# Kernel tuning notes

Hardware: AMD Instinct MI355X
Metric: run time of the kernel (lower is better)

## Reference

```python
import jax, jax.numpy as jnp
import numpy as np

DIM = 768
HEADS = 12
HEAD_DIM = DIM // HEADS
SCALE = HEAD_DIM ** -0.5


def setup_inputs() -> dict:
    key = jax.random.key(0)
    k1, k2, k3, k4, k5 = jax.random.split(key, 5)
    B, N = 4, 2048
    x = jax.random.normal(k1, (B, N, DIM), dtype=jnp.float32)
    # qkv Linear: weight [3*dim, dim], bias [3*dim]
    w_qkv = jax.random.normal(k2, (3 * DIM, DIM), dtype=jnp.float32) * (DIM ** -0.5)
    b_qkv = jax.random.normal(k3, (3 * DIM,), dtype=jnp.float32) * 0.01
    # proj Linear: weight [dim, dim], bias [dim]
    w_proj = jax.random.normal(k4, (DIM, DIM), dtype=jnp.float32) * (DIM ** -0.5)
    b_proj = jax.random.normal(k5, (DIM,), dtype=jnp.float32) * 0.01
    return {"x": x, "w_qkv": w_qkv, "b_qkv": b_qkv, "w_proj": w_proj, "b_proj": b_proj}


def reference(x, w_qkv, b_qkv, w_proj, b_proj):
    B, N, C = x.shape
    qkv = (jnp.einsum('bnc,oc->bno', x, w_qkv) + b_qkv)
    qkv = qkv.reshape(B, N, 3, HEADS, HEAD_DIM).transpose(2, 0, 3, 1, 4)
    q, k, v = qkv[0], qkv[1], qkv[2]
    attn = jnp.einsum('bhqd,bhkd->bhqk', q, k) * SCALE
    attn = jax.nn.softmax(attn, axis=-1)
    out = jnp.einsum('bhqk,bhkd->bhqd', attn, v)  # [B, H, N, Dh]
    out = out.transpose(0, 2, 1, 3).reshape(B, N, C)
    # dropout is identity in eval mode
    return jnp.einsum('bnc,oc->bno', out, w_proj) + b_proj
```

## Files before the change

kernel.cpp:

```cpp
#include <hip/hip_runtime.h>
#include <hip/hip_bf16.h>

using bf16 = __hip_bfloat16;
typedef __bf16 bf16x8 __attribute__((ext_vector_type(8)));
typedef short short4v __attribute__((ext_vector_type(4)));
typedef short short8v __attribute__((ext_vector_type(8)));
typedef float float4v __attribute__((ext_vector_type(4)));

#define DIM   768
#define NH    12
#define HD    64
#define SEQ   2048
#define BATCH 4
#define TOK   (BATCH * SEQ)
#define SCALE_QL2E 0.18033688011112042f

#define NX  (TOK * DIM)
#define NWQ (3 * DIM * DIM)
#define NWP (DIM * DIM)

__device__ __forceinline__ short f2bf(float f) {
  union { bf16 h; short s; } u;
  u.h = __float2bfloat16(f);
  return u.s;
}

union frag8 { short4v h[2]; short8v s; bf16x8 b; unsigned u[4]; };

__device__ __forceinline__ void async_copy16(const bf16* g, short* l) {
  __builtin_amdgcn_global_load_lds(
      (const __attribute__((address_space(1))) unsigned int*)g,
      (__attribute__((address_space(3))) unsigned int*)l, 16, 0, 0);
}
__device__ __forceinline__ void async_copy4(const bf16* g, short* l) {
  __builtin_amdgcn_global_load_lds(
      (const __attribute__((address_space(1))) unsigned int*)g,
      (__attribute__((address_space(3))) unsigned int*)l, 4, 0, 0);
}

#define BARRIER __builtin_amdgcn_s_barrier()
#define LGKM0 asm volatile("s_waitcnt lgkmcnt(0)" ::: "memory")
#define VW0 asm volatile("s_waitcnt vmcnt(0)" ::: "memory")
#define NOSTG (void)0
#define NOVW  (void)0

__global__ void __launch_bounds__(256)
cvt3(const float* __restrict__ a, bf16* __restrict__ oa, long na,
     const float* __restrict__ b, bf16* __restrict__ ob, long nb,
     const float* __restrict__ c, bf16* __restrict__ oc, long nc) {
  const long i = ((long)blockIdx.x * 256 + threadIdx.x) * 8;
  const float* src; bf16* dst; long off;
  if (i < na)                { src = a; dst = oa; off = i; }
  else if (i < na + nb)      { src = b; dst = ob; off = i - na; }
  else if (i < na + nb + nc) { src = c; dst = oc; off = i - na - nb; }
  else return;
  const float4v x0 = *(const float4v*)(src + off);
  const float4v x1 = *(const float4v*)(src + off + 4);
  short8v r;
  r[0] = f2bf(x0[0]); r[1] = f2bf(x0[1]); r[2] = f2bf(x0[2]); r[3] = f2bf(x0[3]);
  r[4] = f2bf(x1[0]); r[5] = f2bf(x1[1]); r[6] = f2bf(x1[2]); r[7] = f2bf(x1[3]);
  *(short8v*)(dst + off) = r;
}

__device__ __forceinline__ void gemm_mainloop(const bf16* __restrict__ A,
                                              const bf16* __restrict__ B,
                                              short* As, short* Bs,
                                              float4v acc[4][4]) {
  const int t = threadIdx.x;
  const int w = t >> 6, l = t & 63, lr = l & 15, q = l >> 4;
  const int wr = ((w >> 1) << 6), wc = ((w & 1) << 6);

  const bf16* Ag = A + (t >> 2) * DIM + (t & 3) * 8;
  const bf16* Bg = B + (t >> 2) * DIM + (t & 3) * 8;

  for (int k0 = 0; k0 < DIM; k0 += 32) {
    __syncthreads();
    async_copy16(Ag,            &As[t * 8]);
    async_copy16(Ag + 64 * DIM, &As[2048 + t * 8]);
    async_copy16(Bg,            &Bs[t * 8]);
    async_copy16(Bg + 64 * DIM, &Bs[2048 + t * 8]);
    Ag += 32; Bg += 32;
    __syncthreads();

    bf16x8 af[4], bfv[4];
#pragma unroll
    for (int i = 0; i < 4; ++i)
      af[i] = *(const bf16x8*)&As[(wr + i * 16 + lr) * 32 + q * 8];
#pragma unroll
    for (int j = 0; j < 4; ++j)
      bfv[j] = *(const bf16x8*)&Bs[(wc + j * 16 + lr) * 32 + q * 8];
#pragma unroll
    for (int i = 0; i < 4; ++i)
#pragma unroll
      for (int j = 0; j < 4; ++j)
        acc[i][j] = __builtin_amdgcn_mfma_f32_16x16x32_bf16(af[i], bfv[j],
                                                            acc[i][j], 0, 0, 0);
  }
}

#define STGP(s, p)                                                            \
  async_copy16(pa + (p) * 32,             &As[s][t * 8]);                     \
  async_copy16(pa + 64 * DIM + (p) * 32,  &As[s][2048 + t * 8]);              \
  async_copy16(pb + (p) * 32,             &Bs[s][t * 8]);                     \
  async_copy16(pb + 64 * DIM + (p) * 32,  &Bs[s][2048 + t * 8]);              \
  async_copy16(pb + 128 * DIM + (p) * 32, &Bs[s][4096 + t * 8]);              \
  async_copy16(pb + 192 * DIM + (p) * 32, &Bs[s][6144 + t * 8]);              \
  async_copy4 (pb3 + (p) * 32,            &Bs[s][8192 + t * 2]);              \
  async_copy4 (pb3 + 16 * DIM + (p) * 32, &Bs[s][8704 + t * 2])

#define PHASE(CUR, STG_, VW_) {                                               \
  bf16x8 af[4], bfv[9];                                                       \
  _Pragma("unroll") for (int mf_ = 0; mf_ < 4; ++mf_)                         \
    af[mf_] = *(const bf16x8*)&As[CUR][mf_ * 512 + arow];                     \
  _Pragma("unroll") for (int nf_ = 0; nf_ < 9; ++nf_)                         \
    bfv[nf_] = *(const bf16x8*)&Bs[CUR][nf_ * 512 + brow];                    \
  STG_; BARRIER; LGKM0;                                                       \
  __builtin_amdgcn_s_setprio(1);                                              \
  _Pragma("unroll") for (int mf_ = 0; mf_ < 4; ++mf_)                         \
  _Pragma("unroll") for (int nf_ = 0; nf_ < 9; ++nf_)                         \
    acc[mf_][nf_] = __builtin_amdgcn_mfma_f32_16x16x32_bf16(                  \
        af[mf_], bfv[nf_], acc[mf_][nf_], 0, 0, 0);                           \
  __builtin_amdgcn_s_setprio(0); VW_; BARRIER; }

__global__ void __launch_bounds__(256, 2)
gemm_qkv(const bf16* __restrict__ X, const bf16* __restrict__ W,
         const float* __restrict__ bias,
         bf16* __restrict__ qb, bf16* __restrict__ kb, bf16* __restrict__ vb) {
  __shared__ short As[2][128 * 32];
  __shared__ short Bs[2][288 * 32];
  const int t = threadIdx.x;
  const int w = t >> 6, l = t & 63, lr = l & 15, q = l >> 4;
  const int wm = w >> 1, wn = w & 1;

  const int orig = blockIdx.x;
  const int swz = (orig & 7) * 64 + (orig >> 3);
  const int tm = swz >> 3, tn = swz & 7;
  const int row0 = tm * 128, col0 = tn * 288;

  const int sr = t >> 2;
  const int scol = (((t & 3) << 3) ^ (((sr >> 1) & 3) << 3));
  const bf16* pa  = X + (size_t)(row0 + sr) * DIM + scol;
  const bf16* pb  = W + (size_t)(col0 + sr) * DIM + scol;
  const int r3 = t >> 4;
  const int c3 = ((t & 15) << 1) ^ (((r3 >> 1) & 3) << 3);
  const bf16* pb3 = W + (size_t)(col0 + 256 + r3) * DIM + c3;

  const int acol = ((q << 3) ^ (((lr >> 1) & 3) << 3));
  const int arow = (wm * 64 + lr) * 32 + acol;
  const int brow = (wn * 144 + lr) * 32 + acol;

  float4v acc[4][9] = {};

  STGP(0, 0);
  VW0; BARRIER;

#pragma unroll 1
  for (int k = 0; k < 22; k += 2) {
    PHASE(0, STGP(1, k + 1), VW0)
    PHASE(1, STGP(0, k + 2), VW0)
  }
  PHASE(0, STGP(1, 23), VW0)
  PHASE(1, NOSTG,       NOVW)

#pragma unroll
  for (int nf = 0; nf < 9; ++nf) {
    const int gn = col0 + wn * 144 + nf * 16 + lr;
    const int which = gn / DIM;
    const int cc = gn - which * DIM;
    const int hh = cc >> 6, dd = cc & 63;
    const float bv = bias[gn];
#pragma unroll
    for (int mf = 0; mf < 4; ++mf) {
      const int gm0 = row0 + wm * 64 + mf * 16 + (q << 2);
      const int b = gm0 >> 11, n0 = gm0 & 2047;
      if (which == 2) {
        short4v pv;
#pragma unroll
        for (int r = 0; r < 4; ++r) pv[r] = f2bf(acc[mf][nf][r] + bv);
        *(short4v*)&vb[((size_t)(b * NH + hh) * HD + dd) * SEQ + n0] = pv;
      } else {
        bf16* dst = (which == 0) ? qb : kb;
        const float sc = (which == 0) ? SCALE_QL2E : 1.0f;
#pragma unroll
        for (int r = 0; r < 4; ++r)
          dst[((size_t)(b * NH + hh) * SEQ + n0 + r) * HD + dd] =
              __float2bfloat16((acc[mf][nf][r] + bv) * sc);
      }
    }
  }
}

#define STG_KV(bb, k1)                                                        \
  async_copy16(Kb + (size_t)((k1) + drow) * HD + skey,       &KV[bb][t * 8]); \
  async_copy16(Kb + (size_t)((k1) + 32 + drow) * HD + skey,  &KV[bb][2048 + t * 8]); \
  async_copy16(Vb + (size_t)drow * SEQ + (k1) + skey,        &KV[bb][4096 + t * 8]); \
  async_copy16(Vb + (size_t)(32 + drow) * SEQ + (k1) + skey, &KV[bb][6144 + t * 8])

#define S_STEP(BK_) {                                                         \
  const short* Bf_ = KV[BK_];                                                 \
  __builtin_amdgcn_s_setprio(1);                                              \
  _Pragma("unroll") for (int jn = 0; jn < 4; ++jn) {                          \
    bf16x8 kf[2];                                                             \
    _Pragma("unroll") for (int kq = 0; kq < 2; ++kq)                          \
      kf[kq] = *(const bf16x8*)&Bf_[(jn * 16 + lr) * 64 +                     \
                                    (((kq * 32) + (q << 3)) ^ key8)];         \
    _Pragma("unroll") for (int it = 0; it < 2; ++it)                          \
    _Pragma("unroll") for (int kq = 0; kq < 2; ++kq)                          \
      s[jn][it] = __builtin_amdgcn_mfma_f32_16x16x32_bf16(kf[kq],             \
                      qf[it][kq], s[jn][it], 0, 0, 0);                        \
  }                                                                           \
  __builtin_amdgcn_s_setprio(0); }

#define PV_STEP(PF_, BP_) {                                                   \
  const short* Bv_ = KV[BP_] + 4096;                                          \
  __builtin_amdgcn_s_setprio(1);                                              \
  _Pragma("unroll") for (int c4 = 0; c4 < 2; ++c4) {                          \
    _Pragma("unroll") for (int dj = 0; dj < 4; ++dj) {                        \
      frag8 vf;                                                               \
      vf.h[0] = *(const short4v*)&Bv_[(dj * 16 + lr) * 64 +                   \
                                      ((c4 * 32 + (q << 2)) ^ key8)];         \
      vf.h[1] = *(const short4v*)&Bv_[(dj * 16 + lr) * 64 +                   \
                                      ((c4 * 32 + 16 + (q << 2)) ^ key8)];    \
      _Pragma("unroll") for (int it = 0; it < 2; ++it)                        \
        o[it][dj] = __builtin_amdgcn_mfma_f32_16x16x32_bf16(PF_[c4][it].b,    \
                        vf.b, o[it][dj], 0, 0, 0);                            \
    }                                                                         \
    _Pragma("unroll") for (int it = 0; it < 2; ++it)                          \
      lacc[it] = __builtin_amdgcn_mfma_f32_16x16x32_bf16(PF_[c4][it].b,       \
                     ones.b, lacc[it], 0, 0, 0);                              \
  }                                                                           \
  __builtin_amdgcn_s_setprio(0); }

#define SM_STEP(PF_)                                                          \
  _Pragma("unroll") for (int it = 0; it < 2; ++it)                            \
  _Pragma("unroll") for (int c4 = 0; c4 < 2; ++c4)                            \
  _Pragma("unroll") for (int r = 0; r < 4; ++r) {                             \
    PF_[c4][it].s[r]     = f2bf(__builtin_amdgcn_exp2f(s[2 * c4][it][r]));    \
    PF_[c4][it].s[4 + r] = f2bf(__builtin_amdgcn_exp2f(s[2 * c4 + 1][it][r]));\
  }

#define FA_BODY(BK_, BP_, BN_, PFP_, PFC_, TILE1_) {                          \
  float4v s[4][2] = {};                                                       \
  S_STEP(BK_);                                                                \
  PV_STEP(PFP_, BP_);                                                         \
  STG_KV(BN_, (TILE1_) * 64);                                                 \
  SM_STEP(PFC_);                                                              \
  VW0; BARRIER; }

__global__ void __launch_bounds__(256, 3)
flash_attn(const bf16* __restrict__ Qp, const bf16* __restrict__ Kp,
           const bf16* __restrict__ Vtp, bf16* __restrict__ Op) {
  const int bh = blockIdx.y, qt = blockIdx.x;
  const int t = threadIdx.x, w = t >> 6, l = t & 63, lr = l & 15, q = l >> 4;
  __shared__ short KV[3][8192];

  const bf16* Qb = Qp  + (size_t)(bh * SEQ + qt * 128) * HD;
  const bf16* Kb = Kp  + (size_t)bh * SEQ * HD;
  const bf16* Vb = Vtp + (size_t)bh * HD * SEQ;

  const int drow = t >> 3;
  const int skey = (((t & 7) ^ drow) & 7) * 8;

  bf16x8 qf[2][2];
#pragma unroll
  for (int it = 0; it < 2; ++it)
#pragma unroll
    for (int kq = 0; kq < 2; ++kq)
      qf[it][kq] = *(const bf16x8*)(Qb + (size_t)(w * 32 + it * 16 + lr) * HD +
                                    kq * 32 + q * 8);

  const int key8 = (lr & 7) << 3;

  frag8 ones;
#pragma unroll
  for (int r = 0; r < 8; ++r) ones.s[r] = (short)0x3F80;

  float4v o[2][4] = {};
  float4v lacc[2] = {};
  frag8 pfA[2][2], pfB[2][2];

  STG_KV(0, 0);
  VW0; BARRIER;

  {
    float4v s[4][2] = {};
    S_STEP(0);
    STG_KV(1, 64);
    SM_STEP(pfA);
    VW0; BARRIER;
  }

  int bK = 1;
#pragma unroll 1
  for (int kt = 1; kt < 31; kt += 2) {
    const int bP = (bK == 0) ? 2 : bK - 1;
    const int bN = (bK == 2) ? 0 : bK + 1;
    FA_BODY(bK, bP, bN, pfA, pfB, kt + 1)
    FA_BODY(bN, bK, bP, pfB, pfA, kt + 2)
    bK = bP;
  }

  {
    float4v s[4][2] = {};
    S_STEP(1);
    PV_STEP(pfA, 0);
    SM_STEP(pfB);
    PV_STEP(pfB, 1);
  }

  const int b = bh / NH, h = bh - b * NH;
#pragma unroll
  for (int it = 0; it < 2; ++it)
#pragma unroll
    for (int r = 0; r < 4; ++r) {
      const float linv = 1.0f / lacc[it][r];
      const int grow = b * SEQ + qt * 128 + w * 32 + it * 16 + (q << 2) + r;
      bf16* orow = Op + (size_t)grow * DIM + h * HD;
#pragma unroll
      for (int dj = 0; dj < 4; ++dj)
        orow[dj * 16 + lr] = __float2bfloat16(o[it][dj][r] * linv);
    }
}

__global__ void __launch_bounds__(256)
gemm_proj(const bf16* __restrict__ A, const bf16* __restrict__ W,
          const float* __restrict__ bias, float* __restrict__ out) {
  __shared__ short As[128 * 32];
  __shared__ short Bs[128 * 32];
  const int t = threadIdx.x;
  const int w = t >> 6, l = t & 63, lr = l & 15, q = l >> 4;
  const int wr = ((w >> 1) << 6), wc = ((w & 1) << 6);
  const int row0 = blockIdx.y * 128, col0 = blockIdx.x * 128;

  float4v acc[4][4] = {};
  gemm_mainloop(A + row0 * DIM, W + col0 * DIM, As, Bs, acc);

#pragma unroll
  for (int j = 0; j < 4; ++j) {
    const int gn = col0 + wc + j * 16 + lr;
    const float bv = bias[gn];
#pragma unroll
    for (int i = 0; i < 4; ++i) {
#pragma unroll
      for (int r = 0; r < 4; ++r) {
        const int gm = row0 + wr + i * 16 + (q << 2) + r;
        out[(size_t)gm * DIM + gn] = acc[i][j][r] + bv;
      }
    }
  }
}

extern "C" void kernel_launch(void* const* d_in, const int* in_sizes, int n_in,
                              void* d_out, int out_size, void* d_ws, size_t ws_size,
                              hipStream_t stream) {
  const float* x      = (const float*)d_in[0];
  const float* w_qkv  = (const float*)d_in[1];
  const float* b_qkv  = (const float*)d_in[2];
  const float* w_proj = (const float*)d_in[3];
  const float* b_proj = (const float*)d_in[4];
  float* out = (float*)d_out;

  const size_t perbuf = (size_t)BATCH * NH * SEQ * HD;
  bf16* qb  = (bf16*)d_ws;
  bf16* kb  = qb + perbuf;
  bf16* vb  = kb + perbuf;
  bf16* ao  = vb + perbuf;
  bf16* xb  = ao + perbuf;
  bf16* wqb = xb + (size_t)NX;
  bf16* wpb = wqb + (size_t)NWQ;

  const int cvt_blocks = (NX + NWQ + NWP) / 8 / 256;
  cvt3<<<cvt_blocks, 256, 0, stream>>>(x, xb, NX, w_qkv, wqb, NWQ, w_proj, wpb, NWP);
  gemm_qkv <<<dim3(512), 256, 0, stream>>>(xb, wqb, b_qkv, qb, kb, vb);
  flash_attn<<<dim3(SEQ / 128, BATCH * NH), 256, 0, stream>>>(qb, kb, vb, ao);
  gemm_proj <<<dim3(DIM / 128, TOK / 128),  256, 0, stream>>>(ao, wpb, b_proj, out);
}
```

Baseline: 203.2 us.

## Rewrite projection GEMM with double-buffered pipeline, 64x192 tiles and swizzled grid

Replaces the single-buffered 128x128 projection GEMM mainloop with a double-buffered async-copy pipeline, reusing the pattern already used by the QKV GEMM. Tiles become 64x192 with an XOR-swizzled LDS layout to avoid bank conflicts, and blocks are remapped so co-scheduled blocks share tiles. Launch bounds request two blocks per CU. The goal is to hide global-load latency and raise occupancy for a kernel that is a small part of total time, at the cost of more complex indexing and more LDS per block.

```diff
diff --git a/kernel.cpp b/kernel.cpp
--- a/kernel.cpp
+++ b/kernel.cpp
@@ -60,42 +60,6 @@
   r[0] = f2bf(x0[0]); r[1] = f2bf(x0[1]); r[2] = f2bf(x0[2]); r[3] = f2bf(x0[3]);
   r[4] = f2bf(x1[0]); r[5] = f2bf(x1[1]); r[6] = f2bf(x1[2]); r[7] = f2bf(x1[3]);
   *(short8v*)(dst + off) = r;
-}
-
-__device__ __forceinline__ void gemm_mainloop(const bf16* __restrict__ A,
-                                              const bf16* __restrict__ B,
-                                              short* As, short* Bs,
-                                              float4v acc[4][4]) {
-  const int t = threadIdx.x;
-  const int w = t >> 6, l = t & 63, lr = l & 15, q = l >> 4;
-  const int wr = ((w >> 1) << 6), wc = ((w & 1) << 6);
-
-  const bf16* Ag = A + (t >> 2) * DIM + (t & 3) * 8;
-  const bf16* Bg = B + (t >> 2) * DIM + (t & 3) * 8;
-
-  for (int k0 = 0; k0 < DIM; k0 += 32) {
-    __syncthreads();
-    async_copy16(Ag,            &As[t * 8]);
-    async_copy16(Ag + 64 * DIM, &As[2048 + t * 8]);
-    async_copy16(Bg,            &Bs[t * 8]);
-    async_copy16(Bg + 64 * DIM, &Bs[2048 + t * 8]);
-    Ag += 32; Bg += 32;
-    __syncthreads();
-
-    bf16x8 af[4], bfv[4];
-#pragma unroll
-    for (int i = 0; i < 4; ++i)
-      af[i] = *(const bf16x8*)&As[(wr + i * 16 + lr) * 32 + q * 8];
-#pragma unroll
-    for (int j = 0; j < 4; ++j)
-      bfv[j] = *(const bf16x8*)&Bs[(wc + j * 16 + lr) * 32 + q * 8];
-#pragma unroll
-    for (int i = 0; i < 4; ++i)
-#pragma unroll
-      for (int j = 0; j < 4; ++j)
-        acc[i][j] = __builtin_amdgcn_mfma_f32_16x16x32_bf16(af[i], bfv[j],
-                                                            acc[i][j], 0, 0, 0);
-  }
 }
 
 #define STGP(s, p)                                                            \
@@ -322,29 +286,72 @@
     }
 }
 
-__global__ void __launch_bounds__(256)
+#define PRJ_STG(s, p)                                                         \
+  async_copy16(pa + (p) * 32,             &Asp[s][t * 8]);                    \
+  async_copy16(pb + (p) * 32,             &Bsp[s][t * 8]);                    \
+  async_copy16(pb + 64 * DIM + (p) * 32,  &Bsp[s][2048 + t * 8]);             \
+  async_copy16(pb + 128 * DIM + (p) * 32, &Bsp[s][4096 + t * 8])
+
+#define PRJ_PHASE(CUR, STG_, VW_) {                                           \
+  bf16x8 af[2], bfv[6];                                                       \
+  _Pragma("unroll") for (int mf_ = 0; mf_ < 2; ++mf_)                         \
+    af[mf_] = *(const bf16x8*)&Asp[CUR][mf_ * 512 + arow];                    \
+  _Pragma("unroll") for (int nf_ = 0; nf_ < 6; ++nf_)                         \
+    bfv[nf_] = *(const bf16x8*)&Bsp[CUR][nf_ * 512 + brow];                   \
+  STG_; BARRIER; LGKM0;                                                       \
+  __builtin_amdgcn_s_setprio(1);                                              \
+  _Pragma("unroll") for (int mf_ = 0; mf_ < 2; ++mf_)                         \
+  _Pragma("unroll") for (int nf_ = 0; nf_ < 6; ++nf_)                         \
+    acc[mf_][nf_] = __builtin_amdgcn_mfma_f32_16x16x32_bf16(                  \
+        af[mf_], bfv[nf_], acc[mf_][nf_], 0, 0, 0);                           \
+  __builtin_amdgcn_s_setprio(0); VW_; BARRIER; }
+
+__global__ void __launch_bounds__(256, 2)
 gemm_proj(const bf16* __restrict__ A, const bf16* __restrict__ W,
           const float* __restrict__ bias, float* __restrict__ out) {
-  __shared__ short As[128 * 32];
-  __shared__ short Bs[128 * 32];
+  __shared__ short Asp[2][64 * 32];
+  __shared__ short Bsp[2][192 * 32];
   const int t = threadIdx.x;
   const int w = t >> 6, l = t & 63, lr = l & 15, q = l >> 4;
-  const int wr = ((w >> 1) << 6), wc = ((w & 1) << 6);
-  const int row0 = blockIdx.y * 128, col0 = blockIdx.x * 128;
-
-  float4v acc[4][4] = {};
-  gemm_mainloop(A + row0 * DIM, W + col0 * DIM, As, Bs, acc);
-
-#pragma unroll
-  for (int j = 0; j < 4; ++j) {
-    const int gn = col0 + wc + j * 16 + lr;
+  const int wm = w >> 1, wn = w & 1;
+
+  const int orig = blockIdx.x;
+  const int swz = (orig & 7) * 64 + (orig >> 3);
+  const int tm = swz >> 2, tn = swz & 3;
+  const int row0 = tm * 64, col0 = tn * 192;
+
+  const int sr = t >> 2;
+  const int scol = (((t & 3) << 3) ^ (((sr >> 1) & 3) << 3));
+  const bf16* pa = A + (size_t)(row0 + sr) * DIM + scol;
+  const bf16* pb = W + (size_t)(col0 + sr) * DIM + scol;
+
+  const int acol = ((q << 3) ^ (((lr >> 1) & 3) << 3));
+  const int arow = (wm * 32 + lr) * 32 + acol;
+  const int brow = (wn * 96 + lr) * 32 + acol;
+
+  float4v acc[2][6] = {};
+
+  PRJ_STG(0, 0);
+  VW0; BARRIER;
+
+#pragma unroll 1
+  for (int k = 0; k < 22; k += 2) {
+    PRJ_PHASE(0, PRJ_STG(1, k + 1), VW0)
+    PRJ_PHASE(1, PRJ_STG(0, k + 2), VW0)
+  }
+  PRJ_PHASE(0, PRJ_STG(1, 23), VW0)
+  PRJ_PHASE(1, NOSTG,          NOVW)
+
+#pragma unroll
+  for (int nf = 0; nf < 6; ++nf) {
+    const int gn = col0 + wn * 96 + nf * 16 + lr;
     const float bv = bias[gn];
 #pragma unroll
-    for (int i = 0; i < 4; ++i) {
+    for (int mf = 0; mf < 2; ++mf) {
 #pragma unroll
       for (int r = 0; r < 4; ++r) {
-        const int gm = row0 + wr + i * 16 + (q << 2) + r;
-        out[(size_t)gm * DIM + gn] = acc[i][j][r] + bv;
+        const int gm = row0 + wm * 32 + mf * 16 + (q << 2) + r;
+        out[(size_t)gm * DIM + gn] = acc[mf][nf][r] + bv;
       }
     }
   }
@@ -373,5 +380,5 @@
   cvt3<<<cvt_blocks, 256, 0, stream>>>(x, xb, NX, w_qkv, wqb, NWQ, w_proj, wpb, NWP);
   gemm_qkv <<<dim3(512), 256, 0, stream>>>(xb, wqb, b_qkv, qb, kb, vb);
   flash_attn<<<dim3(SEQ / 128, BATCH * NH), 256, 0, stream>>>(qb, kb, vb, ao);
-  gemm_proj <<<dim3(DIM / 128, TOK / 128),  256, 0, stream>>>(ao, wpb, b_proj, out);
-}
+  gemm_proj <<<dim3(512), 256, 0, stream>>>(ao, wpb, b_proj, out);
+}
```

New measurement: 196.2 us, median of 3. 1.04x faster.
